# Performance work log

Hardware: AMD Instinct MI355X
Metric: run time of the kernel (lower is better)

Reference implementation:

```python
import jax, jax.numpy as jnp
import numpy as np

IN_CH = 128
HID = 64
EPS = 1e-5
N_NODES = 20000
E_UND = 80000


def _build_line_graph(edge_index, num_nodes):
    # dedupe to unique undirected edges (src<dst); line-graph nodes = these edges
    src = np.asarray(edge_index[0]); dst = np.asarray(edge_index[1])
    m = src < dst
    u, v = src[m], dst[m]
    key = u.astype(np.int64) * num_nodes + v.astype(np.int64)
    _, first = np.unique(key, return_index=True)
    u, v = u[first], v[first]
    E = u.shape[0]
    # incidence lists grouped by node; all ordered pairs of co-incident edges
    nodes = np.concatenate([u, v])
    eids = np.concatenate([np.arange(E), np.arange(E)])
    order = np.argsort(nodes, kind="stable")
    nodes_s, eids_s = nodes[order], eids[order]
    counts = np.bincount(nodes_s, minlength=num_nodes)
    offsets = np.concatenate([np.zeros(1, np.int64), np.cumsum(counts)])
    grp_start = offsets[nodes_s]
    reps = counts[nodes_s]
    total = int(reps.sum())
    starts = np.cumsum(reps) - reps
    idx = np.arange(total) - np.repeat(starts, reps) + np.repeat(grp_start, reps)
    row = np.repeat(eids_s, reps); col = eids_s[idx]
    keep = row != col
    return np.stack([u, v]), np.stack([row[keep], col[keep]])


def _gcn_conv(x, src, dst, W, b):
    # PyG GCNConv: add self loops, symmetric D^-1/2 (A+I) D^-1/2 normalization
    N = x.shape[0]
    sl = jnp.arange(N)
    s = jnp.concatenate([src, sl]); d = jnp.concatenate([dst, sl])
    deg = jax.ops.segment_sum(jnp.ones(s.shape[0], x.dtype), d, num_segments=N)
    dinv = jax.lax.rsqrt(jnp.maximum(deg, 1.0))
    h = x @ W
    msg = h[s] * (dinv[s] * dinv[d])[:, None]
    return jax.ops.segment_sum(msg, d, num_segments=N) + b


def _edge_scores(line_x, lsrc, ldst, W1, b1, gamma1, beta1, W2, b2):
    h = _gcn_conv(line_x, lsrc, ldst, W1, b1)
    mu = h.mean(0); var = h.var(0)  # BatchNorm1d, training-mode batch stats
    h = jax.nn.relu(gamma1 * (h - mu) * jax.lax.rsqrt(var + EPS) + beta1)
    return jax.nn.sigmoid(_gcn_conv(h, lsrc, ldst, W2, b2))[:, 0]


def _cluster(clean, topk_idx, num_nodes):
    ti = np.asarray(topk_idx)
    sel_src = np.asarray(clean[0])[ti]; sel_dst = np.asarray(clean[1])[ti]
    n2c = np.arange(num_nodes)
    rev = sel_dst[::-1]
    _, fi = np.unique(rev, return_index=True)
    last = sel_dst.shape[0] - 1 - fi
    n2c[sel_dst[last]] = sel_src[last]
    uniq = np.unique(n2c)
    M = int(uniq.shape[0])
    old_to_new = np.full(num_nodes, -1, np.int64)
    old_to_new[uniq] = np.arange(M)
    return old_to_new[n2c], uniq, M


def _make_graph():
    rng = np.random.default_rng(0)
    a = rng.integers(0, N_NODES, E_UND)
    off = rng.integers(1, N_NODES, E_UND)
    b = (a + off) % N_NODES  # no self loops
    u = np.minimum(a, b); v = np.maximum(a, b)
    return np.stack([np.concatenate([u, v]), np.concatenate([v, u])]).astype(np.int64)


def _make_params():
    ks = jax.random.split(jax.random.key(0), 4)
    x = jax.random.normal(ks[0], (N_NODES, IN_CH), jnp.float32)
    W1 = jax.random.normal(ks[1], (IN_CH, HID), jnp.float32) / np.float32(np.sqrt(IN_CH))
    b1 = jnp.zeros((HID,), jnp.float32)
    gamma1 = jnp.ones((HID,), jnp.float32)
    beta1 = jnp.zeros((HID,), jnp.float32)
    W2 = jax.random.normal(ks[2], (HID, 1), jnp.float32) / np.float32(np.sqrt(HID))
    b2 = jnp.zeros((1,), jnp.float32)
    return x, W1, b1, gamma1, beta1, W2, b2


def setup_inputs() -> dict:
    x, W1, b1, gamma1, beta1, W2, b2 = _make_params()
    return {
        "x": x, "W1": W1, "b1": b1, "gamma1": gamma1, "beta1": beta1,
        "W2": W2, "b2": b2,
        "edge_index": jnp.asarray(_make_graph()),
        "batch": jnp.zeros((N_NODES,), jnp.int32),
    }


def reference(x, W1, b1, gamma1, beta1, W2, b2, edge_index, batch):
    N = x.shape[0]
    clean, line_ei = _build_line_graph(edge_index, N)
    csrc = jnp.asarray(clean[0]); cdst = jnp.asarray(clean[1])
    lsrc = jnp.asarray(line_ei[0]); ldst = jnp.asarray(line_ei[1])
    line_x = 0.5 * (x[csrc] + x[cdst])  # line-graph node features
    scores = _edge_scores(line_x, lsrc, ldst, W1, b1, gamma1, beta1, W2, b2)
    E_c = scores.shape[0]
    k = max(1, min(E_c // 2, N // 2))
    _, topk_idx = jax.lax.top_k(scores, k)
    new_indices, uniq, M = _cluster(clean, topk_idx, N)
    ni = jnp.asarray(new_indices)
    # aggregate: per-cluster mean of member node features (code's weights are unused)
    counts = jax.ops.segment_sum(jnp.ones(N, x.dtype), ni, num_segments=M)
    x_pool = jax.ops.segment_sum(x, ni, num_segments=M) / counts[:, None]
    batch_pool = batch[jnp.asarray(uniq)]
    # build_new_edges: relabel, drop self loops, coalesce (sorted unique)
    ei = np.asarray(edge_index)
    ns = new_indices[ei[0]]; nd = new_indices[ei[1]]
    keep = ns != nd
    pk = ns[keep] * M + nd[keep]
    upk = np.unique(pk)
    edge_index_pool = jnp.asarray(np.stack([upk // M, upk % M]))
    return (x_pool, edge_index_pool, batch_pool, scores, ni)
```

## Files before the change

kernel.cpp:

```cpp
#include <hip/hip_runtime.h>
#include <stdint.h>

typedef unsigned long long u64;
typedef unsigned int u32;

#define NND 20000
#define EUA 160000
#define EFE 80000
#define ICH 128
#define HIDC 64
#define SCAN_BS 256
#define NB_N ((NND + 255) / 256)
#define NB_EU ((EUA + 255) / 256)
#define NB_EF ((EFE + 255) / 256)
#define NB_E64 ((EFE * HIDC + 255) / 256)
#define NB_X ((NND * ICH + 255) / 256)
#define NSCAN_B ((NND + SCAN_BS - 1) / SCAN_BS)
#define HIST_BLOCKS 128
#define GEB 64
#define XS_PAD 132
#define NCHAIN 4096
#define OUT_MAX_INIT 3000000
#define SEL_BINS 4096


__global__ void kScanA(const int* __restrict__ in, int* __restrict__ out,
                       int* __restrict__ bsums, int n) {
    __shared__ int sh[SCAN_BS];
    int tid = threadIdx.x;
    int i = blockIdx.x * SCAN_BS + tid;
    int v = (i < n) ? in[i] : 0;
    sh[tid] = v;
    __syncthreads();
    for (int o = 1; o < SCAN_BS; o <<= 1) {
        int t = (tid >= o) ? sh[tid - o] : 0;
        __syncthreads();
        sh[tid] += t;
        __syncthreads();
    }
    if (i < n) out[i] = sh[tid] - v;
    if (tid == SCAN_BS - 1) bsums[blockIdx.x] = sh[tid];
}
__global__ void kScanB(int* __restrict__ out, const int* __restrict__ bsums,
                       int n, int nb, int* __restrict__ totalDst) {
    __shared__ int sh[160];
    int tid = threadIdx.x;
    if (tid <= nb) sh[tid] = (tid < nb) ? bsums[tid] : 0;
    __syncthreads();
    if (tid == 0) {
        int acc = 0;
        for (int i = 0; i < nb; i++) { int t = sh[i]; sh[i] = acc; acc += t; }
        sh[nb] = acc;
    }
    __syncthreads();
    int i = blockIdx.x * SCAN_BS + tid;
    if (i < n) out[i] += sh[blockIdx.x];
    if (i == 0) {
        int tot = sh[nb];
        out[n] = tot;
        *totalDst = tot;
    }
}

__global__ void kFilterCount(const int* __restrict__ ei, int* __restrict__ cnt) {
    int i = blockIdx.x * 256 + threadIdx.x;
    if (i >= EUA) return;
    int s = ei[i], d = ei[EUA + i];
    if (s < d) atomicAdd(&cnt[s], 1);
}
__global__ void kFilterScatter(const int* __restrict__ ei, const int* __restrict__ offA,
                               int* __restrict__ tmp, int* __restrict__ bucketV) {
    int i = blockIdx.x * 256 + threadIdx.x;
    if (i >= EUA) return;
    int s = ei[i], d = ei[EUA + i];
    if (s < d) {
        int p = offA[s] + atomicAdd(&tmp[s], 1);
        bucketV[p] = d;
    }
}
__global__ void kRankSort(const int* __restrict__ in, int* __restrict__ out,
                          const int* __restrict__ offA, int* __restrict__ ucnt) {
    int a = blockIdx.x;
    int s = offA[a], e = offA[a + 1], len = e - s;
    for (int j = threadIdx.x; j < len; j += 64) {
        int v = in[s + j];
        int r = 0;
        for (int i = 0; i < len; i++) {
            int w = in[s + i];
            r += (w < v) || (w == v && i < j);
        }
        out[s + r] = v;
    }
    __syncthreads();
    int c = 0;
    for (int j = threadIdx.x; j < len; j += 64)
        c += (j == 0) || (out[s + j] != out[s + j - 1]);
#pragma unroll
    for (int o = 32; o > 0; o >>= 1) c += __shfl_down(c, o, 64);
    if (threadIdx.x == 0) ucnt[a] = c;
}
__global__ void kCompactInc(const int* __restrict__ arr, const int* __restrict__ offA,
                            const int* __restrict__ uoff, int* __restrict__ eU,
                            int* __restrict__ eV, int* __restrict__ icnt) {
    int u = blockIdx.x * 256 + threadIdx.x;
    if (u >= NND) return;
    int s = offA[u], e = offA[u + 1], o = uoff[u];
    int myc = 0;
    for (int i = s; i < e; i++)
        if (i == s || arr[i] != arr[i - 1]) {
            int v = arr[i];
            eU[o] = u; eV[o] = v; o++;
            atomicAdd(&icnt[v], 1);
            myc++;
        }
    if (myc) atomicAdd(&icnt[u], myc);
}

__global__ void kIncScatterDinv(const int* __restrict__ eU, const int* __restrict__ eV,
                                const int* __restrict__ scal, const int* __restrict__ ioff,
                                int* __restrict__ itmp, int* __restrict__ ilist,
                                const int* __restrict__ icnt, float* __restrict__ dinv) {
    int e = blockIdx.x * 256 + threadIdx.x;
    if (e >= scal[0]) return;
    int u = eU[e], v = eV[e];
    ilist[ioff[u] + atomicAdd(&itmp[u], 1)] = e;
    ilist[ioff[v] + atomicAdd(&itmp[v], 1)] = e;
    dinv[e] = rsqrtf((float)(icnt[u] + icnt[v] - 1));
}

__global__ void kGemm(const float* __restrict__ x, const float* __restrict__ W1,
                      const int* __restrict__ eU, const int* __restrict__ eV,
                      const int* __restrict__ scal, float* __restrict__ h) {
    __shared__ float W1s[ICH][HIDC];
    __shared__ float xs[GEB][XS_PAD];
    int t = threadIdx.x;
    int E = scal[0];
    int e0 = blockIdx.x * GEB;
    if (e0 >= E) return;

    {
        const float4* Wv = (const float4*)W1;
        float4* Ws = (float4*)&W1s[0][0];
        for (int i = t; i < ICH * HIDC / 4; i += 256) Ws[i] = Wv[i];
    }
    {
        int eb = t >> 2, q = t & 3;
        int e = e0 + eb;
        if (e < E) {
            int u = eU[e], v = eV[e];
            const float4* xu = (const float4*)(x + (size_t)u * ICH) + q * 8;
            const float4* xv = (const float4*)(x + (size_t)v * ICH) + q * 8;
            float* xd = &xs[eb][q * 32];
#pragma unroll
            for (int i = 0; i < 8; i++) {
                float4 a = xu[i], b = xv[i];
                xd[i * 4 + 0] = 0.5f * (a.x + b.x);
                xd[i * 4 + 1] = 0.5f * (a.y + b.y);
                xd[i * 4 + 2] = 0.5f * (a.z + b.z);
                xd[i * 4 + 3] = 0.5f * (a.w + b.w);
            }
        }
    }
    __syncthreads();

    int cg4 = (t & 15) * 4;
    int es = t >> 4;
    float a00=0,a01=0,a02=0,a03=0, a10=0,a11=0,a12=0,a13=0;
    float a20=0,a21=0,a22=0,a23=0, a30=0,a31=0,a32=0,a33=0;
#pragma unroll 4
    for (int k = 0; k < ICH; k++) {
        float4 wv = *(const float4*)&W1s[k][cg4];
        float x0 = xs[es][k], x1 = xs[es + 16][k];
        float x2 = xs[es + 32][k], x3 = xs[es + 48][k];
        a00 += x0 * wv.x; a01 += x0 * wv.y; a02 += x0 * wv.z; a03 += x0 * wv.w;
        a10 += x1 * wv.x; a11 += x1 * wv.y; a12 += x1 * wv.z; a13 += x1 * wv.w;
        a20 += x2 * wv.x; a21 += x2 * wv.y; a22 += x2 * wv.z; a23 += x2 * wv.w;
        a30 += x3 * wv.x; a31 += x3 * wv.y; a32 += x3 * wv.z; a33 += x3 * wv.w;
    }
    int e;
    e = e0 + es;
    if (e < E) *(float4*)&h[(size_t)e * HIDC + cg4] = make_float4(a00, a01, a02, a03);
    e = e0 + es + 16;
    if (e < E) *(float4*)&h[(size_t)e * HIDC + cg4] = make_float4(a10, a11, a12, a13);
    e = e0 + es + 32;
    if (e < E) *(float4*)&h[(size_t)e * HIDC + cg4] = make_float4(a20, a21, a22, a23);
    e = e0 + es + 48;
    if (e < E) *(float4*)&h[(size_t)e * HIDC + cg4] = make_float4(a30, a31, a32, a33);
}

__global__ void kSGather(const float* __restrict__ h, const float* __restrict__ dinv,
                         const int* __restrict__ ioff, const int* __restrict__ ilist,
                         float* __restrict__ S) {
    int n = blockIdx.x;
    int c = threadIdx.x;
    int s = ioff[n], e = ioff[n + 1];
    float acc = 0.f;
    for (int j = s; j < e; j++) {
        int ed = ilist[j];
        acc += h[(size_t)ed * HIDC + c] * dinv[ed];
    }
    S[(size_t)n * HIDC + c] = acc;
}
__global__ void kConv1Red1(const float* __restrict__ h, const float* __restrict__ S,
                           const float* __restrict__ dinv, const int* __restrict__ eU,
                           const int* __restrict__ eV, const float* __restrict__ b1,
                           const int* __restrict__ scal, float* __restrict__ h2,
                           float* __restrict__ partial) {
    int t = threadIdx.x;
    int g = blockIdx.x * 4 + (t >> 6);
    int c = t & 63;
    int E = scal[0];
    float bc = b1[c];
    float acc = 0.f;
    for (int e = g; e < E; e += NCHAIN) {
        float a = dinv[e];
        float v = a * (S[(size_t)eU[e] * HIDC + c] + S[(size_t)eV[e] * HIDC + c]) -
                  a * a * h[(size_t)e * HIDC + c] + bc;
        h2[(size_t)e * HIDC + c] = v;
        acc += v;
    }
    partial[g * HIDC + c] = acc;
}
__global__ void kRed1v(const float* __restrict__ h2, const int* __restrict__ scal,
                       const float* __restrict__ muvar, float* __restrict__ partial) {
    int t = threadIdx.x;
    int g = blockIdx.x * 4 + (t >> 6);
    int c = t & 63;
    int E = scal[0];
    float m = muvar[c];
    float acc = 0.f;
    for (int e = g; e < E; e += NCHAIN) {
        float d = h2[(size_t)e * HIDC + c] - m;
        acc += d * d;
    }
    partial[g * HIDC + c] = acc;
}
__global__ void kRed2(const float* __restrict__ partial, const int* __restrict__ scal,
                      float* __restrict__ muvar, int pass) {
    __shared__ float sh[4][HIDC];
    int t = threadIdx.x;
    int q = t >> 6, c = t & 63;
    float acc = 0.f;
    int g0 = q * (NCHAIN / 4);
    for (int g = g0; g < g0 + NCHAIN / 4; g++) acc += partial[g * HIDC + c];
    sh[q][c] = acc;
    __syncthreads();
    if (q == 0) {
        float s = ((sh[0][c] + sh[1][c]) + sh[2][c]) + sh[3][c];
        muvar[pass * HIDC + c] = s / (float)scal[0];
    }
}
__global__ void kNormZ(const float* __restrict__ h2, const float* __restrict__ muvar,
                       const float* __restrict__ gamma1, const float* __restrict__ beta1,
                       const float* __restrict__ W2, const int* __restrict__ scal,
                       float* __restrict__ z) {
    int idx = blockIdx.x * 256 + threadIdx.x;
    int e = idx >> 6;
    if (e >= scal[0]) return;
    int c = idx & 63;
    float t = gamma1[c] * (h2[idx] - muvar[c]) * rsqrtf(muvar[HIDC + c] + 1e-5f) + beta1[c];
    t = t > 0.f ? t : 0.f;
    float p = t * W2[c];
#pragma unroll
    for (int o = 32; o > 0; o >>= 1) p += __shfl_down(p, o, 64);
    if (c == 0) z[e] = p;
}
__global__ void kS2(const float* __restrict__ z, const float* __restrict__ dinv,
                    const int* __restrict__ ioff, const int* __restrict__ ilist,
                    float* __restrict__ S2) {
    int n = blockIdx.x * 256 + threadIdx.x;
    if (n >= NND) return;
    float acc = 0.f;
    for (int j = ioff[n]; j < ioff[n + 1]; j++) {
        int e = ilist[j];
        acc += z[e] * dinv[e];
    }
    S2[n] = acc;
}
__global__ void kScore(const float* __restrict__ z, const float* __restrict__ S2,
                       const float* __restrict__ dinv, const int* __restrict__ eU,
                       const int* __restrict__ eV, const float* __restrict__ b2,
                       const int* __restrict__ scal, float* __restrict__ score,
                       u64* __restrict__ okey, int* __restrict__ krem,
                       u64* __restrict__ pref, u64* __restrict__ minOkey) {
    int e = blockIdx.x * 256 + threadIdx.x;
    if (e < NND) minOkey[e] = ~0ULL;
    int E = scal[0];
    if (e >= E) return;
    if (e == 0) {
        int k = E / 2;
        if (k > NND / 2) k = NND / 2;
        if (k < 1) k = 1;
        *krem = k;
        *pref = 1ULL << 48;
    }
    float a = dinv[e];
    float l = a * (S2[eU[e]] + S2[eV[e]]) - a * a * z[e] + b2[0];
    float s = 1.f / (1.f + expf(-l));
    score[e] = s;
    u32 b = __float_as_uint(s);
    b = (b >> 31) ? ~b : (b | 0x80000000u);
    okey[e] = (((u64)b) << 17) | (u32)(0x1FFFFu - (u32)e);
}

__global__ void kHist(const u64* __restrict__ okey, const int* __restrict__ scal,
                      int* __restrict__ hist, const u64* __restrict__ pref,
                      u64 maskHi, int shift) {
    __shared__ int sh[4][SEL_BINS];
    int t = threadIdx.x;
    for (int j = t; j < 4 * SEL_BINS; j += 256) ((int*)sh)[j] = 0;
    __syncthreads();
    int wv = t >> 6;
    int E = scal[0];
    u64 p = *pref;
    for (int e = blockIdx.x * 256 + t; e < E; e += HIST_BLOCKS * 256) {
        u64 kk = okey[e];
        if ((kk & maskHi) == p)
            atomicAdd(&sh[wv][(int)((kk >> shift) & (SEL_BINS - 1))], 1);
    }
    __syncthreads();
    for (int j = t; j < SEL_BINS; j += 256) {
        int v = sh[0][j] + sh[1][j] + sh[2][j] + sh[3][j];
        if (v) atomicAdd(&hist[j], v);
    }
}
__global__ void kSelPass(int* __restrict__ hist, u64* __restrict__ pref,
                         int* __restrict__ krem, int shift) {
    __shared__ int sh[SEL_BINS];
    __shared__ int aux[256];
    __shared__ int shKr;
    int t = threadIdx.x;
    int g = 0;
#pragma unroll
    for (int j = 0; j < 16; j++) {
        int v = hist[16 * t + j];
        sh[16 * t + j] = v;
        hist[16 * t + j] = 0;
        g += v;
    }
    if (t == 0) shKr = *krem;
    aux[t] = g;
    __syncthreads();
    for (int o = 1; o < 256; o <<= 1) {
        int v = (t + o < 256) ? aux[t + o] : 0;
        __syncthreads();
        aux[t] += v;
        __syncthreads();
    }
    int kr = shKr;
    int suf = aux[t] - g;
    if (suf < kr && kr <= suf + g) {
        int cum = suf, found = 16 * t;
        for (int b = 16 * t + 15; b >= 16 * t; b--) {
            int hc = sh[b];
            if (cum + hc >= kr) { found = b; break; }
            cum += hc;
        }
        *krem = kr - cum;
        *pref |= ((u64)found) << shift;
    }
}

__global__ void kMinKeyInit(const u64* __restrict__ okey, const int* __restrict__ eV,
                            const int* __restrict__ scal, const u64* __restrict__ pref,
                            u64* __restrict__ minOkey, int* __restrict__ n2c) {
    int i = blockIdx.x * 256 + threadIdx.x;
    if (i < NND) n2c[i] = i;
    if (i < scal[0]) {
        u64 k = okey[i];
        if (k >= *pref) atomicMin(&minOkey[eV[i]], k);
    }
}
__global__ void kN2cSet(const u64* __restrict__ okey, const int* __restrict__ eU,
                        const int* __restrict__ eV, const int* __restrict__ scal,
                        const u64* __restrict__ pref, const u64* __restrict__ minOkey,
                        int* __restrict__ n2c) {
    int e = blockIdx.x * 256 + threadIdx.x;
    if (e >= scal[0]) return;
    u64 k = okey[e];
    int v = eV[e];
    if (k >= *pref && k == minOkey[v]) n2c[v] = eU[e];
}
__global__ void kPresent(const int* __restrict__ n2c, int* __restrict__ present) {
    int n = blockIdx.x * 256 + threadIdx.x;
    if (n < NND) present[n2c[n]] = 1;
}

__global__ void kNiXacc(const float* __restrict__ x, const int* __restrict__ n2c,
                        const int* __restrict__ o2n, int* __restrict__ ni,
                        int* __restrict__ ccnt, float* __restrict__ dout) {
    int idx = blockIdx.x * 256 + threadIdx.x;
    if (idx >= NND * ICH) return;
    int n = idx >> 7, c = idx & 127;
    int m = o2n[n2c[n]];
    atomicAdd(&dout[(size_t)m * ICH + c], x[idx]);
    if (c == 0) {
        ni[n] = m;
        atomicAdd(&ccnt[m], 1);
    }
}
__global__ void kXdiv(float* __restrict__ dout, const int* __restrict__ ccnt,
                      const int* __restrict__ scal) {
    int idx = blockIdx.x * 256 + threadIdx.x;
    int m = idx >> 7;
    if (m >= scal[2]) return;
    dout[idx] /= (float)ccnt[m];
}

__global__ void kCEcount(const int* __restrict__ ei, const int* __restrict__ ni,
                         int* __restrict__ ecnt2) {
    int i = blockIdx.x * 256 + threadIdx.x;
    if (i >= EUA) return;
    int a = ni[ei[i]], b = ni[ei[EUA + i]];
    if (a != b) atomicAdd(&ecnt2[a], 1);
}
__global__ void kCEscatter(const int* __restrict__ ei, const int* __restrict__ ni,
                           const int* __restrict__ eoff2, int* __restrict__ etmp2,
                           int* __restrict__ bkD) {
    int i = blockIdx.x * 256 + threadIdx.x;
    if (i >= EUA) return;
    int a = ni[ei[i]], b = ni[ei[EUA + i]];
    if (a != b) {
        int p = eoff2[a] + atomicAdd(&etmp2[a], 1);
        bkD[p] = b;
    }
}
__global__ void kCEwriteTail(const int* __restrict__ bkD2, const int* __restrict__ eoff2,
                             const int* __restrict__ ueoff, const int* __restrict__ scal,
                             const int* __restrict__ batch, const int* __restrict__ present,
                             const int* __restrict__ o2n, const float* __restrict__ score,
                             const int* __restrict__ ni, float* __restrict__ dout) {
    int i = blockIdx.x * 256 + threadIdx.x;
    int E = scal[0], M = scal[2], Ep = scal[3];
    size_t base = (size_t)M * ICH;
    if (i < NND) {
        int s = eoff2[i], e = eoff2[i + 1];
        float* r0 = dout + base;
        float* r1 = r0 + Ep;
        int o = ueoff[i];
        for (int j = s; j < e; j++)
            if (j == s || bkD2[j] != bkD2[j - 1]) {
                r0[o] = (float)i;
                r1[o] = (float)bkD2[j];
                o++;
            }
    }
    size_t tb = base + 2 * (size_t)Ep;
    if (i < NND && present[i]) dout[tb + o2n[i]] = (float)batch[i];
    if (i < E) dout[tb + M + i] = score[i];
    if (i < NND) dout[tb + M + E + i] = (float)ni[i];
}

extern "C" void kernel_launch(void* const* d_in, const int* in_sizes, int n_in,
                              void* d_out, int out_size, void* d_ws, size_t ws_size,
                              hipStream_t stream) {
    (void)in_sizes; (void)n_in; (void)ws_size;
    const float* x = (const float*)d_in[0];
    const float* W1 = (const float*)d_in[1];
    const float* b1 = (const float*)d_in[2];
    const float* gamma1 = (const float*)d_in[3];
    const float* beta1 = (const float*)d_in[4];
    const float* W2 = (const float*)d_in[5];
    const float* b2 = (const float*)d_in[6];
    const int* ei = (const int*)d_in[7];
    const int* batch = (const int*)d_in[8];
    float* dout = (float*)d_out;

    char* w = (char*)d_ws;
    size_t off = 0;
    auto carve = [&](size_t bytes) -> void* {
        off = (off + 255) & ~(size_t)255;
        void* p = w + off;
        off += bytes;
        return p;
    };
    char* zero0 = w;
    int* cnt = (int*)carve(NND * 4);
    int* tmp = (int*)carve(NND * 4);
    int* icnt = (int*)carve(NND * 4);
    int* itmp = (int*)carve(NND * 4);
    int* present = (int*)carve(NND * 4);
    int* ccnt = (int*)carve(NND * 4);
    int* ecnt2 = (int*)carve(NND * 4);
    int* etmp2 = (int*)carve(NND * 4);
    int* scal = (int*)carve(16 * 4);
    int* hist = (int*)carve(SEL_BINS * 4);
    size_t zeroBytes = off;
    int* offA = (int*)carve((NND + 2) * 4);
    int* ucnt = (int*)carve(NND * 4);
    int* uoff = (int*)carve((NND + 2) * 4);
    int* ioff = (int*)carve((NND + 2) * 4);
    int* bsums = (int*)carve((NSCAN_B + 2) * 4);
    int* n2c = (int*)carve(NND * 4);
    int* o2n = (int*)carve((NND + 2) * 4);
    int* niArr = (int*)carve(NND * 4);
    int* eoff2 = (int*)carve((NND + 2) * 4);
    int* uecnt = (int*)carve(NND * 4);
    int* ueoff = (int*)carve((NND + 2) * 4);
    int* bucketV = (int*)carve(EUA * 4);
    int* bucketS = (int*)carve(EUA * 4);
    int* eU = (int*)carve(EFE * 4);
    int* eV = (int*)carve(EFE * 4);
    int* ilist = (int*)carve(2 * EFE * 4);
    int* ilistS = (int*)carve(2 * EFE * 4);
    int* bkD = (int*)carve(EUA * 4);
    int* bkD2 = (int*)carve(EUA * 4);
    u64* okey = (u64*)carve(EFE * 8);
    u64* minOkey = (u64*)carve(NND * 8);
    u64* dpref = (u64*)carve(8);
    float* dinv = (float*)carve(EFE * 4);
    float* h = (float*)carve((size_t)EFE * HIDC * 4);
    float* h2 = (float*)carve((size_t)EFE * HIDC * 4);
    float* Snode = (float*)carve((size_t)NND * HIDC * 4);
    float* partial = (float*)carve((size_t)NCHAIN * HIDC * 4);
    float* muvar = (float*)carve(128 * 4);
    float* zArr = (float*)carve(EFE * 4);
    float* S2 = (float*)carve(NND * 4);
    float* score = (float*)carve(EFE * 4);

    auto scan = [&](const int* in, int* outp, int* totalDst) {
        kScanA<<<NSCAN_B, SCAN_BS, 0, stream>>>(in, outp, bsums, NND);
        kScanB<<<NSCAN_B, SCAN_BS, 0, stream>>>(outp, bsums, NND, NSCAN_B, totalDst);
    };

    size_t outInit = (size_t)out_size;
    if (outInit > OUT_MAX_INIT) outInit = OUT_MAX_INIT;
    hipMemsetAsync(zero0, 0, zeroBytes, stream);
    hipMemsetAsync(d_out, 0, outInit * 4, stream);

    kFilterCount<<<NB_EU, 256, 0, stream>>>(ei, cnt);
    scan(cnt, offA, scal + 15);
    kFilterScatter<<<NB_EU, 256, 0, stream>>>(ei, offA, tmp, bucketV);
    kRankSort<<<NND, 64, 0, stream>>>(bucketV, bucketS, offA, ucnt);
    scan(ucnt, uoff, scal + 0);
    kCompactInc<<<NB_N, 256, 0, stream>>>(bucketS, offA, uoff, eU, eV, icnt);

    scan(icnt, ioff, scal + 15);
    kIncScatterDinv<<<NB_EF, 256, 0, stream>>>(eU, eV, scal, ioff, itmp, ilist, icnt, dinv);
    kRankSort<<<NND, 64, 0, stream>>>(ilist, ilistS, ioff, tmp);

    kGemm<<<(EFE + GEB - 1) / GEB, 256, 0, stream>>>(x, W1, eU, eV, scal, h);
    kSGather<<<NND, HIDC, 0, stream>>>(h, dinv, ioff, ilistS, Snode);
    kConv1Red1<<<NCHAIN / 4, 256, 0, stream>>>(h, Snode, dinv, eU, eV, b1, scal, h2, partial);
    kRed2<<<1, 256, 0, stream>>>(partial, scal, muvar, 0);
    kRed1v<<<NCHAIN / 4, 256, 0, stream>>>(h2, scal, muvar, partial);
    kRed2<<<1, 256, 0, stream>>>(partial, scal, muvar, 1);
    kNormZ<<<NB_E64, 256, 0, stream>>>(h2, muvar, gamma1, beta1, W2, scal, zArr);

    kS2<<<NB_N, 256, 0, stream>>>(zArr, dinv, ioff, ilistS, S2);
    kScore<<<NB_EF, 256, 0, stream>>>(zArr, S2, dinv, eU, eV, b2, scal, score, okey,
                                      scal + 1, dpref, minOkey);

    for (int p = 0; p < 4; p++) {
        int shift = 36 - 12 * p;
        u64 maskHi = (~0ULL) << (shift + 12);
        kHist<<<HIST_BLOCKS, 256, 0, stream>>>(okey, scal, hist, dpref, maskHi, shift);
        kSelPass<<<1, 256, 0, stream>>>(hist, dpref, scal + 1, shift);
    }

    kMinKeyInit<<<NB_EF, 256, 0, stream>>>(okey, eV, scal, dpref, minOkey, n2c);
    kN2cSet<<<NB_EF, 256, 0, stream>>>(okey, eU, eV, scal, dpref, minOkey, n2c);
    kPresent<<<NB_N, 256, 0, stream>>>(n2c, present);
    scan(present, o2n, scal + 2);
    kNiXacc<<<NB_X, 256, 0, stream>>>(x, n2c, o2n, niArr, ccnt, dout);
    kXdiv<<<NB_X, 256, 0, stream>>>(dout, ccnt, scal);

    kCEcount<<<NB_EU, 256, 0, stream>>>(ei, niArr, ecnt2);
    scan(ecnt2, eoff2, scal + 4);
    kCEscatter<<<NB_EU, 256, 0, stream>>>(ei, niArr, eoff2, etmp2, bkD);
    kRankSort<<<NND, 64, 0, stream>>>(bkD, bkD2, eoff2, uecnt);
    scan(uecnt, ueoff, scal + 3);
    kCEwriteTail<<<NB_EF, 256, 0, stream>>>(bkD2, eoff2, ueoff, scal, batch, present,
                                            o2n, score, niArr, dout);
}
```

Baseline: 412.6 us.

## Use fixed 64-slot buckets, 16-bit radix select, and fuse divide with edge count

Replaces the count-scan-scatter CSR builds for node adjacency and incidence lists with fixed 64-entry per-node buckets filled by atomics. This removes two count kernels and two scans. The top-k radix select now uses 16-bit digits with packed 16-bit shared counters, which cuts four histogram/select passes to three. The mean division is fused with the coarse edge count kernel. It assumes every node has at most 64 incident edges, grows the bucket memory, and makes the single-block select pass scan a much larger histogram.

```diff
diff --git a/kernel.cpp b/kernel.cpp
--- a/kernel.cpp
+++ b/kernel.cpp
@@ -21,7 +21,7 @@
 #define XS_PAD 132
 #define NCHAIN 4096
 #define OUT_MAX_INIT 3000000
-#define SEL_BINS 4096
+#define BK64 64
 
 
 __global__ void kScanA(const int* __restrict__ in, int* __restrict__ out,
@@ -62,49 +62,44 @@
     }
 }
 
-__global__ void kFilterCount(const int* __restrict__ ei, int* __restrict__ cnt) {
-    int i = blockIdx.x * 256 + threadIdx.x;
-    if (i >= EUA) return;
-    int s = ei[i], d = ei[EUA + i];
-    if (s < d) atomicAdd(&cnt[s], 1);
-}
-__global__ void kFilterScatter(const int* __restrict__ ei, const int* __restrict__ offA,
-                               int* __restrict__ tmp, int* __restrict__ bucketV) {
+__global__ void kFilterScatter64(const int* __restrict__ ei, int* __restrict__ cnt,
+                                 int* __restrict__ bucketV) {
     int i = blockIdx.x * 256 + threadIdx.x;
     if (i >= EUA) return;
     int s = ei[i], d = ei[EUA + i];
     if (s < d) {
-        int p = offA[s] + atomicAdd(&tmp[s], 1);
-        bucketV[p] = d;
-    }
-}
-__global__ void kRankSort(const int* __restrict__ in, int* __restrict__ out,
-                          const int* __restrict__ offA, int* __restrict__ ucnt) {
+        int p = atomicAdd(&cnt[s], 1);
+        bucketV[(s << 6) + p] = d;
+    }
+}
+__global__ void kRankSort64(const int* __restrict__ in, int* __restrict__ out,
+                            const int* __restrict__ lenA, int* __restrict__ ucnt) {
     int a = blockIdx.x;
-    int s = offA[a], e = offA[a + 1], len = e - s;
+    int len = lenA[a];
+    int base = a << 6;
     for (int j = threadIdx.x; j < len; j += 64) {
-        int v = in[s + j];
+        int v = in[base + j];
         int r = 0;
         for (int i = 0; i < len; i++) {
-            int w = in[s + i];
+            int w = in[base + i];
             r += (w < v) || (w == v && i < j);
         }
-        out[s + r] = v;
+        out[base + r] = v;
     }
     __syncthreads();
     int c = 0;
     for (int j = threadIdx.x; j < len; j += 64)
-        c += (j == 0) || (out[s + j] != out[s + j - 1]);
+        c += (j == 0) || (out[base + j] != out[base + j - 1]);
 #pragma unroll
     for (int o = 32; o > 0; o >>= 1) c += __shfl_down(c, o, 64);
     if (threadIdx.x == 0) ucnt[a] = c;
 }
-__global__ void kCompactInc(const int* __restrict__ arr, const int* __restrict__ offA,
+__global__ void kCompactInc(const int* __restrict__ arr, const int* __restrict__ cnt,
                             const int* __restrict__ uoff, int* __restrict__ eU,
                             int* __restrict__ eV, int* __restrict__ icnt) {
     int u = blockIdx.x * 256 + threadIdx.x;
     if (u >= NND) return;
-    int s = offA[u], e = offA[u + 1], o = uoff[u];
+    int s = u << 6, e = s + cnt[u], o = uoff[u];
     int myc = 0;
     for (int i = s; i < e; i++)
         if (i == s || arr[i] != arr[i - 1]) {
@@ -116,15 +111,15 @@
     if (myc) atomicAdd(&icnt[u], myc);
 }
 
-__global__ void kIncScatterDinv(const int* __restrict__ eU, const int* __restrict__ eV,
-                                const int* __restrict__ scal, const int* __restrict__ ioff,
-                                int* __restrict__ itmp, int* __restrict__ ilist,
-                                const int* __restrict__ icnt, float* __restrict__ dinv) {
+__global__ void kIncScatterDinv64(const int* __restrict__ eU, const int* __restrict__ eV,
+                                  const int* __restrict__ scal, int* __restrict__ itmp,
+                                  int* __restrict__ ilist, const int* __restrict__ icnt,
+                                  float* __restrict__ dinv) {
     int e = blockIdx.x * 256 + threadIdx.x;
     if (e >= scal[0]) return;
     int u = eU[e], v = eV[e];
-    ilist[ioff[u] + atomicAdd(&itmp[u], 1)] = e;
-    ilist[ioff[v] + atomicAdd(&itmp[v], 1)] = e;
+    ilist[(u << 6) + atomicAdd(&itmp[u], 1)] = e;
+    ilist[(v << 6) + atomicAdd(&itmp[v], 1)] = e;
     dinv[e] = rsqrtf((float)(icnt[u] + icnt[v] - 1));
 }
 
@@ -189,14 +184,14 @@
 }
 
 __global__ void kSGather(const float* __restrict__ h, const float* __restrict__ dinv,
-                         const int* __restrict__ ioff, const int* __restrict__ ilist,
+                         const int* __restrict__ icnt, const int* __restrict__ ilist,
                          float* __restrict__ S) {
     int n = blockIdx.x;
     int c = threadIdx.x;
-    int s = ioff[n], e = ioff[n + 1];
+    int base = n << 6, len = icnt[n];
     float acc = 0.f;
-    for (int j = s; j < e; j++) {
-        int ed = ilist[j];
+    for (int j = 0; j < len; j++) {
+        int ed = ilist[base + j];
         acc += h[(size_t)ed * HIDC + c] * dinv[ed];
     }
     S[(size_t)n * HIDC + c] = acc;
@@ -266,13 +261,14 @@
     if (c == 0) z[e] = p;
 }
 __global__ void kS2(const float* __restrict__ z, const float* __restrict__ dinv,
-                    const int* __restrict__ ioff, const int* __restrict__ ilist,
+                    const int* __restrict__ icnt, const int* __restrict__ ilist,
                     float* __restrict__ S2) {
     int n = blockIdx.x * 256 + threadIdx.x;
     if (n >= NND) return;
+    int base = n << 6, len = icnt[n];
     float acc = 0.f;
-    for (int j = ioff[n]; j < ioff[n + 1]; j++) {
-        int e = ilist[j];
+    for (int j = 0; j < len; j++) {
+        int e = ilist[base + j];
         acc += z[e] * dinv[e];
     }
     S2[n] = acc;
@@ -303,41 +299,40 @@
     okey[e] = (((u64)b) << 17) | (u32)(0x1FFFFu - (u32)e);
 }
 
-__global__ void kHist(const u64* __restrict__ okey, const int* __restrict__ scal,
-                      int* __restrict__ hist, const u64* __restrict__ pref,
-                      u64 maskHi, int shift) {
-    __shared__ int sh[4][SEL_BINS];
+__global__ void kHist16(const u64* __restrict__ okey, const int* __restrict__ scal,
+                        u32* __restrict__ hist, const u64* __restrict__ pref,
+                        u64 maskHi, int shift) {
+    __shared__ u32 sh[32768];
     int t = threadIdx.x;
-    for (int j = t; j < 4 * SEL_BINS; j += 256) ((int*)sh)[j] = 0;
-    __syncthreads();
-    int wv = t >> 6;
+    for (int j = t; j < 32768; j += 256) sh[j] = 0;
+    __syncthreads();
     int E = scal[0];
     u64 p = *pref;
     for (int e = blockIdx.x * 256 + t; e < E; e += HIST_BLOCKS * 256) {
         u64 kk = okey[e];
-        if ((kk & maskHi) == p)
-            atomicAdd(&sh[wv][(int)((kk >> shift) & (SEL_BINS - 1))], 1);
-    }
-    __syncthreads();
-    for (int j = t; j < SEL_BINS; j += 256) {
-        int v = sh[0][j] + sh[1][j] + sh[2][j] + sh[3][j];
-        if (v) atomicAdd(&hist[j], v);
-    }
-}
-__global__ void kSelPass(int* __restrict__ hist, u64* __restrict__ pref,
-                         int* __restrict__ krem, int shift) {
-    __shared__ int sh[SEL_BINS];
+        if ((kk & maskHi) == p) {
+            int bin = (int)((kk >> shift) & 0xFFFF);
+            atomicAdd(&sh[bin >> 1], 1u << ((bin & 1) << 4));
+        }
+    }
+    __syncthreads();
+    for (int j = t; j < 32768; j += 256) {
+        u32 v = sh[j];
+        if (v) {
+            u32 lo = v & 0xFFFFu, hi = v >> 16;
+            if (lo) atomicAdd(&hist[2 * j], lo);
+            if (hi) atomicAdd(&hist[2 * j + 1], hi);
+        }
+    }
+}
+__global__ void kSelPass16(u32* __restrict__ hist, u64* __restrict__ pref,
+                           int* __restrict__ krem, int shift) {
     __shared__ int aux[256];
     __shared__ int shKr;
     int t = threadIdx.x;
+    int base = t * 256;
     int g = 0;
-#pragma unroll
-    for (int j = 0; j < 16; j++) {
-        int v = hist[16 * t + j];
-        sh[16 * t + j] = v;
-        hist[16 * t + j] = 0;
-        g += v;
-    }
+    for (int j = 0; j < 256; j++) g += (int)hist[base + j];
     if (t == 0) shKr = *krem;
     aux[t] = g;
     __syncthreads();
@@ -350,15 +345,17 @@
     int kr = shKr;
     int suf = aux[t] - g;
     if (suf < kr && kr <= suf + g) {
-        int cum = suf, found = 16 * t;
-        for (int b = 16 * t + 15; b >= 16 * t; b--) {
-            int hc = sh[b];
+        int cum = suf, found = base;
+        for (int b = base + 255; b >= base; b--) {
+            int hc = (int)hist[b];
             if (cum + hc >= kr) { found = b; break; }
             cum += hc;
         }
         *krem = kr - cum;
         *pref |= ((u64)found) << shift;
     }
+    __syncthreads();
+    for (int j = 0; j < 256; j++) hist[base + j] = 0;
 }
 
 __global__ void kMinKeyInit(const u64* __restrict__ okey, const int* __restrict__ eV,
@@ -399,21 +396,17 @@
         atomicAdd(&ccnt[m], 1);
     }
 }
-__global__ void kXdiv(float* __restrict__ dout, const int* __restrict__ ccnt,
-                      const int* __restrict__ scal) {
+__global__ void kXdivCEcount(float* __restrict__ dout, const int* __restrict__ ccnt,
+                             const int* __restrict__ scal, const int* __restrict__ ei,
+                             const int* __restrict__ ni, int* __restrict__ ecnt2) {
     int idx = blockIdx.x * 256 + threadIdx.x;
-    int m = idx >> 7;
-    if (m >= scal[2]) return;
-    dout[idx] /= (float)ccnt[m];
-}
-
-__global__ void kCEcount(const int* __restrict__ ei, const int* __restrict__ ni,
-                         int* __restrict__ ecnt2) {
-    int i = blockIdx.x * 256 + threadIdx.x;
-    if (i >= EUA) return;
-    int a = ni[ei[i]], b = ni[ei[EUA + i]];
-    if (a != b) atomicAdd(&ecnt2[a], 1);
-}
+    if (idx < scal[2] * ICH) dout[idx] /= (float)ccnt[idx >> 7];
+    if (idx < EUA) {
+        int a = ni[ei[idx]], b = ni[ei[EUA + idx]];
+        if (a != b) atomicAdd(&ecnt2[a], 1);
+    }
+}
+
 __global__ void kCEscatter(const int* __restrict__ ei, const int* __restrict__ ni,
                            const int* __restrict__ eoff2, int* __restrict__ etmp2,
                            int* __restrict__ bkD) {
@@ -424,6 +417,27 @@
         int p = eoff2[a] + atomicAdd(&etmp2[a], 1);
         bkD[p] = b;
     }
+}
+__global__ void kRankSort(const int* __restrict__ in, int* __restrict__ out,
+                          const int* __restrict__ offA, int* __restrict__ ucnt) {
+    int a = blockIdx.x;
+    int s = offA[a], e = offA[a + 1], len = e - s;
+    for (int j = threadIdx.x; j < len; j += 64) {
+        int v = in[s + j];
+        int r = 0;
+        for (int i = 0; i < len; i++) {
+            int w = in[s + i];
+            r += (w < v) || (w == v && i < j);
+        }
+        out[s + r] = v;
+    }
+    __syncthreads();
+    int c = 0;
+    for (int j = threadIdx.x; j < len; j += 64)
+        c += (j == 0) || (out[s + j] != out[s + j - 1]);
+#pragma unroll
+    for (int o = 32; o > 0; o >>= 1) c += __shfl_down(c, o, 64);
+    if (threadIdx.x == 0) ucnt[a] = c;
 }
 __global__ void kCEwriteTail(const int* __restrict__ bkD2, const int* __restrict__ eoff2,
                              const int* __restrict__ ueoff, const int* __restrict__ scal,
@@ -476,20 +490,17 @@
     };
     char* zero0 = w;
     int* cnt = (int*)carve(NND * 4);
-    int* tmp = (int*)carve(NND * 4);
+    int* itmp = (int*)carve(NND * 4);
     int* icnt = (int*)carve(NND * 4);
-    int* itmp = (int*)carve(NND * 4);
     int* present = (int*)carve(NND * 4);
     int* ccnt = (int*)carve(NND * 4);
     int* ecnt2 = (int*)carve(NND * 4);
     int* etmp2 = (int*)carve(NND * 4);
     int* scal = (int*)carve(16 * 4);
-    int* hist = (int*)carve(SEL_BINS * 4);
+    u32* hist = (u32*)carve(65536 * 4);
     size_t zeroBytes = off;
-    int* offA = (int*)carve((NND + 2) * 4);
     int* ucnt = (int*)carve(NND * 4);
     int* uoff = (int*)carve((NND + 2) * 4);
-    int* ioff = (int*)carve((NND + 2) * 4);
     int* bsums = (int*)carve((NSCAN_B + 2) * 4);
     int* n2c = (int*)carve(NND * 4);
     int* o2n = (int*)carve((NND + 2) * 4);
@@ -497,12 +508,12 @@
     int* eoff2 = (int*)carve((NND + 2) * 4);
     int* uecnt = (int*)carve(NND * 4);
     int* ueoff = (int*)carve((NND + 2) * 4);
-    int* bucketV = (int*)carve(EUA * 4);
-    int* bucketS = (int*)carve(EUA * 4);
+    int* bucketV = (int*)carve((size_t)NND * BK64 * 4);
+    int* bucketS = (int*)carve((size_t)NND * BK64 * 4);
     int* eU = (int*)carve(EFE * 4);
     int* eV = (int*)carve(EFE * 4);
-    int* ilist = (int*)carve(2 * EFE * 4);
-    int* ilistS = (int*)carve(2 * EFE * 4);
+    int* ilist = (int*)carve((size_t)NND * BK64 * 4);
+    int* ilistS = (int*)carve((size_t)NND * BK64 * 4);
     int* bkD = (int*)carve(EUA * 4);
     int* bkD2 = (int*)carve(EUA * 4);
     u64* okey = (u64*)carve(EFE * 8);
@@ -528,34 +539,31 @@
     hipMemsetAsync(zero0, 0, zeroBytes, stream);
     hipMemsetAsync(d_out, 0, outInit * 4, stream);
 
-    kFilterCount<<<NB_EU, 256, 0, stream>>>(ei, cnt);
-    scan(cnt, offA, scal + 15);
-    kFilterScatter<<<NB_EU, 256, 0, stream>>>(ei, offA, tmp, bucketV);
-    kRankSort<<<NND, 64, 0, stream>>>(bucketV, bucketS, offA, ucnt);
+    kFilterScatter64<<<NB_EU, 256, 0, stream>>>(ei, cnt, bucketV);
+    kRankSort64<<<NND, 64, 0, stream>>>(bucketV, bucketS, cnt, ucnt);
     scan(ucnt, uoff, scal + 0);
-    kCompactInc<<<NB_N, 256, 0, stream>>>(bucketS, offA, uoff, eU, eV, icnt);
-
-    scan(icnt, ioff, scal + 15);
-    kIncScatterDinv<<<NB_EF, 256, 0, stream>>>(eU, eV, scal, ioff, itmp, ilist, icnt, dinv);
-    kRankSort<<<NND, 64, 0, stream>>>(ilist, ilistS, ioff, tmp);
+    kCompactInc<<<NB_N, 256, 0, stream>>>(bucketS, cnt, uoff, eU, eV, icnt);
+
+    kIncScatterDinv64<<<NB_EF, 256, 0, stream>>>(eU, eV, scal, itmp, ilist, icnt, dinv);
+    kRankSort64<<<NND, 64, 0, stream>>>(ilist, ilistS, icnt, ucnt);
 
     kGemm<<<(EFE + GEB - 1) / GEB, 256, 0, stream>>>(x, W1, eU, eV, scal, h);
-    kSGather<<<NND, HIDC, 0, stream>>>(h, dinv, ioff, ilistS, Snode);
+    kSGather<<<NND, HIDC, 0, stream>>>(h, dinv, icnt, ilistS, Snode);
     kConv1Red1<<<NCHAIN / 4, 256, 0, stream>>>(h, Snode, dinv, eU, eV, b1, scal, h2, partial);
     kRed2<<<1, 256, 0, stream>>>(partial, scal, muvar, 0);
     kRed1v<<<NCHAIN / 4, 256, 0, stream>>>(h2, scal, muvar, partial);
     kRed2<<<1, 256, 0, stream>>>(partial, scal, muvar, 1);
     kNormZ<<<NB_E64, 256, 0, stream>>>(h2, muvar, gamma1, beta1, W2, scal, zArr);
 
-    kS2<<<NB_N, 256, 0, stream>>>(zArr, dinv, ioff, ilistS, S2);
+    kS2<<<NB_N, 256, 0, stream>>>(zArr, dinv, icnt, ilistS, S2);
     kScore<<<NB_EF, 256, 0, stream>>>(zArr, S2, dinv, eU, eV, b2, scal, score, okey,
                                       scal + 1, dpref, minOkey);
 
-    for (int p = 0; p < 4; p++) {
-        int shift = 36 - 12 * p;
-        u64 maskHi = (~0ULL) << (shift + 12);
-        kHist<<<HIST_BLOCKS, 256, 0, stream>>>(okey, scal, hist, dpref, maskHi, shift);
-        kSelPass<<<1, 256, 0, stream>>>(hist, dpref, scal + 1, shift);
+    for (int p = 0; p < 3; p++) {
+        int shift = 32 - 16 * p;
+        u64 maskHi = (~0ULL) << (shift + 16);
+        kHist16<<<HIST_BLOCKS, 256, 0, stream>>>(okey, scal, hist, dpref, maskHi, shift);
+        kSelPass16<<<1, 256, 0, stream>>>(hist, dpref, scal + 1, shift);
     }
 
     kMinKeyInit<<<NB_EF, 256, 0, stream>>>(okey, eV, scal, dpref, minOkey, n2c);
@@ -563,9 +571,8 @@
     kPresent<<<NB_N, 256, 0, stream>>>(n2c, present);
     scan(present, o2n, scal + 2);
     kNiXacc<<<NB_X, 256, 0, stream>>>(x, n2c, o2n, niArr, ccnt, dout);
-    kXdiv<<<NB_X, 256, 0, stream>>>(dout, ccnt, scal);
-
-    kCEcount<<<NB_EU, 256, 0, stream>>>(ei, niArr, ecnt2);
+    kXdivCEcount<<<NB_X, 256, 0, stream>>>(dout, ccnt, scal, ei, niArr, ecnt2);
+
     scan(ecnt2, eoff2, scal + 4);
     kCEscatter<<<NB_EU, 256, 0, stream>>>(ei, niArr, eoff2, etmp2, bkD);
     kRankSort<<<NND, 64, 0, stream>>>(bkD, bkD2, eoff2, uecnt);
```

Result: slower. 479.1 us (+16.1%).
